# Performance work log

Hardware: AMD Instinct MI355X
Metric: run time of the kernel (lower is better)

## Reference

```python
import jax, jax.numpy as jnp
import numpy as np

TEMPERATURE = 1.0  # spec.temperature, clamped to >=1e-6 in the original
NEG_INF = -1000000000.0


def setup_inputs() -> dict:
    key = jax.random.key(0)
    k_x, k_w1, k_b1, k_w2, k_b2 = jax.random.split(key, 5)
    N, d_in, d_h, E = 32768, 1024, 256, 64
    s1 = 1.0 / np.sqrt(d_in)
    s2 = 1.0 / np.sqrt(d_h)
    return {
        "stage_input": jax.random.normal(k_x, (N, d_in), dtype=jnp.float32),
        "w1": jax.random.uniform(k_w1, (d_in, d_h), jnp.float32, -s1, s1),
        "b1": jax.random.uniform(k_b1, (d_h,), jnp.float32, -s1, s1),
        "w2": jax.random.uniform(k_w2, (d_h, E), jnp.float32, -s2, s2),
        "b2": jax.random.uniform(k_b2, (E,), jnp.float32, -s2, s2),
        "top_k": 8,
    }


def reference(stage_input, w1, b1, w2, b2, top_k):
    # Router MLP: Linear -> ReLU -> (Dropout, eval=identity) -> Linear
    h = jax.nn.relu(stage_input @ w1 + b1)          # [N, d_hidden]
    logits = h @ w2 + b2                             # [N, E]

    scaled = logits / TEMPERATURE
    E = scaled.shape[-1]
    k = min(int(top_k), E)
    if 0 < k < E:
        vals, idx = jax.lax.top_k(scaled, k)         # [N, k]
        rows = jnp.arange(scaled.shape[0])[:, None]
        masked = jnp.full_like(scaled, NEG_INF).at[rows, idx].set(vals)
    else:
        masked = scaled

    probs = jax.nn.softmax(masked, axis=-1)          # [N, E]
    return logits, masked, probs
```

## Files before the change

### kernel.cpp

```cpp
#include <hip/hip_runtime.h>
#include <hip/hip_bf16.h>
#include <float.h>


#define N_ROWS 32768
#define D_IN   1024
#define D_H    256
#define N_E    64
#define NEG_INF_VAL (-1000000000.0f)

typedef _Float16 f16x8 __attribute__((ext_vector_type(8)));
typedef float    f32x4  __attribute__((ext_vector_type(4)));
typedef float    f32x16 __attribute__((ext_vector_type(16)));

#define MM32(A, B, C) __builtin_amdgcn_mfma_f32_32x32x16_f16(A, B, C, 0, 0, 0)
#define MM16(A, B, C) __builtin_amdgcn_mfma_f32_16x16x32_f16(A, B, C, 0, 0, 0)

#define KBAR()                                         \
  do {                                                 \
    asm volatile("s_waitcnt lgkmcnt(0)" ::: "memory"); \
    __builtin_amdgcn_s_barrier();                      \
    asm volatile("" ::: "memory");                     \
  } while (0)

__global__ __launch_bounds__(256) void split_weights_kernel(
    const float* __restrict__ w1, const float* __restrict__ w2,
    _Float16* __restrict__ w1pk_h, _Float16* __restrict__ w1pk_l,
    _Float16* __restrict__ w2pk_h, _Float16* __restrict__ w2pk_l) {
  int idx = blockIdx.x * 256 + threadIdx.x;
  if (idx < D_IN * D_H) {
    const int k = idx >> 8;
    const int n = idx & 255;
    const float v = w1[idx];
    const _Float16 hi = (_Float16)v;
    const _Float16 lo = (_Float16)(v - (float)hi);
    const int wv8 = n >> 5, l31 = n & 31;
    const int it = k >> 6, kf = (k >> 4) & 3, kg = (k >> 3) & 1, j = k & 7;
    const int lane = kg * 32 + l31;
    const int off = (((wv8 * 16 + it) * 4 + kf) * 64 + lane) * 8 + j;
    w1pk_h[off] = hi;
    w1pk_l[off] = lo;
  } else {
    idx -= D_IN * D_H;
    const int k = idx >> 6;
    const int e = idx & 63;
    const float v = w2[idx];
    const _Float16 hi = (_Float16)v;
    const _Float16 lo = (_Float16)(v - (float)hi);
    const int s = k >> 5, kg = (k >> 3) & 3, j = k & 7;
    const int f = e >> 4, cc = e & 15;
    const int lane = kg * 16 + cc;
    const int off = ((s * 4 + f) * 64 + lane) * 8 + j;
    w2pk_h[off] = hi;
    w2pk_l[off] = lo;
  }
}

__global__ __launch_bounds__(512, 2) void fused_router_kernel(
    const float* __restrict__ x, const _Float16* __restrict__ w1pk_h,
    const _Float16* __restrict__ w1pk_l, const float* __restrict__ b1,
    const _Float16* __restrict__ w2pk_h, const _Float16* __restrict__ w2pk_l,
    const float* __restrict__ b2, const int* __restrict__ topk_p,
    float* __restrict__ out_logits, float* __restrict__ out_masked,
    float* __restrict__ out_probs) {
  __shared__ char lds[65536];

  const int t  = threadIdx.x;
  const int m0 = blockIdx.x * 64;

  const int srow = t >> 3;
  const int slot = (t & 7) * 16;
  const int sw   = (srow & 7) << 4;

  const int wv   = t >> 6;
  const int lane = t & 63;
  const int l31  = lane & 31;
  const int kg   = lane >> 5;

  const float* xrowp = x + (size_t)(m0 + srow) * D_IN + (t & 7) * 8;
  const f16x8* bph = (const f16x8*)w1pk_h;
  const f16x8* bpl = (const f16x8*)w1pk_l;

  f32x16 acc0, acc1;
#pragma unroll
  for (int i = 0; i < 16; ++i) { acc0[i] = 0.f; acc1[i] = 0.f; }

  f16x8 uh0, uh1, uh2, uh3, ul0, ul1, ul2, ul3;
  f16x8 vh0, vh1, vh2, vh3, vl0, vl1, vl2, vl3;

#define STAGE_WRITE(bufi, q0, q1)                                            \
  do {                                                                       \
    const float vv[8] = {q0.x, q0.y, q0.z, q0.w, q1.x, q1.y, q1.z, q1.w};    \
    f16x8 hi8, lo8;                                                          \
    _Pragma("unroll") for (int j = 0; j < 8; ++j) {                          \
      const _Float16 hv = (_Float16)vv[j];                                   \
      hi8[j] = hv; lo8[j] = (_Float16)(vv[j] - (float)hv);                   \
    }                                                                        \
    char* bb = lds + (bufi) * 16384 + srow * 256;                            \
    *(f16x8*)(bb + (slot ^ sw)) = hi8;                                       \
    *(f16x8*)(bb + 128 + (slot ^ sw)) = lo8;                                 \
  } while (0)

#define LOAD_B(BH0, BH1, BH2, BH3, BL0, BL1, BL2, BL3, itv)                  \
  do {                                                                       \
    const int ch = (wv * 16 + (itv)) * 256 + lane;                           \
    BH0 = bph[ch + 0 * 64]; BH1 = bph[ch + 1 * 64];                          \
    BH2 = bph[ch + 2 * 64]; BH3 = bph[ch + 3 * 64];                          \
    BL0 = bpl[ch + 0 * 64]; BL1 = bpl[ch + 1 * 64];                          \
    BL2 = bpl[ch + 2 * 64]; BL3 = bpl[ch + 3 * 64];                          \
  } while (0)

#define MFMA_KF(rb, kfv, BH, BL)                                             \
  do {                                                                       \
    const int kb = (kfv) * 32 + kg * 16;                                     \
    const char* ap0 = (rb) + l31 * 256 + (kb ^ ((l31 & 7) << 4));            \
    const char* ap1 = ap0 + 32 * 256;                                        \
    const f16x8 ah0 = *(const f16x8*)(ap0);                                  \
    const f16x8 al0 = *(const f16x8*)(ap0 + 128);                            \
    const f16x8 ah1 = *(const f16x8*)(ap1);                                  \
    const f16x8 al1 = *(const f16x8*)(ap1 + 128);                            \
    acc0 = MM32(al0, BH, acc0); acc1 = MM32(al1, BH, acc1);                  \
    acc0 = MM32(ah0, BL, acc0); acc1 = MM32(ah1, BL, acc1);                  \
    acc0 = MM32(ah0, BH, acc0); acc1 = MM32(ah1, BH, acc1);                  \
  } while (0)

#define GSTEP(ITV, LB, CH0, CH1, CH2, CH3, CL0, CL1, CL2, CL3,               \
              NH0, NH1, NH2, NH3, NL0, NL1, NL2, NL3)                        \
  do {                                                                       \
    float4 p0, p1;                                                           \
    const bool more = (ITV) + 1 < 16;                                        \
    if (more) {                                                              \
      const float4* xp = (const float4*)(xrowp + ((ITV) + 1) * 64);          \
      p0 = xp[0]; p1 = xp[1];                                                \
      LOAD_B(NH0, NH1, NH2, NH3, NL0, NL1, NL2, NL3, (ITV) + 1);             \
    }                                                                        \
    const char* rb = lds + (LB) * 16384;                                     \
    MFMA_KF(rb, 0, CH0, CL0);                                                \
    MFMA_KF(rb, 1, CH1, CL1);                                                \
    MFMA_KF(rb, 2, CH2, CL2);                                                \
    MFMA_KF(rb, 3, CH3, CL3);                                                \
    if (more) STAGE_WRITE(1 - (LB), p0, p1);                                 \
    KBAR();                                                                  \
  } while (0)

  {
    const float4* xp = (const float4*)(xrowp);
    const float4 q0 = xp[0], q1 = xp[1];
    STAGE_WRITE(0, q0, q1);
    LOAD_B(uh0, uh1, uh2, uh3, ul0, ul1, ul2, ul3, 0);
  }
  KBAR();

#pragma unroll
  for (int ii = 0; ii < 8; ++ii) {
    GSTEP(2 * ii, 0, uh0, uh1, uh2, uh3, ul0, ul1, ul2, ul3,
          vh0, vh1, vh2, vh3, vl0, vl1, vl2, vl3);
    GSTEP(2 * ii + 1, 1, vh0, vh1, vh2, vh3, vl0, vl1, vl2, vl3,
          uh0, uh1, uh2, uh3, ul0, ul1, ul2, ul3);
  }

#define EPI(ACC, MF)                                                         \
  do {                                                                       \
    const int colg = wv * 32 + l31;                                          \
    const float bias = b1[colg];                                             \
    _Pragma("unroll") for (int r = 0; r < 16; ++r) {                         \
      const int row = (MF) * 32 + (r & 3) + 8 * (r >> 2) + 4 * kg;           \
      const float hv = fmaxf(ACC[r] + bias, 0.0f);                           \
      const _Float16 hhi = (_Float16)hv;                                     \
      const _Float16 hlo = (_Float16)(hv - (float)hhi);                      \
      const int byo = row * 512 + ((colg * 2) ^ ((row & 7) << 4));           \
      *(_Float16*)(lds + byo) = hhi;                                         \
      *(_Float16*)(lds + 32768 + byo) = hlo;                                 \
    }                                                                        \
  } while (0)

  EPI(acc0, 0); EPI(acc1, 1);
#undef EPI
  KBAR();

  if (wv < 4) {
    const int c   = lane & 15;
    const int kg4 = lane >> 4;
    const int rowl = wv * 16 + c;
    const int sw2 = (rowl & 7) << 4;
    const char* hhb = lds + rowl * 512;
    const char* hlb = lds + 32768 + rowl * 512;
    const f16x8* b2ph = (const f16x8*)w2pk_h;
    const f16x8* b2pl = (const f16x8*)w2pk_l;

    f32x4 r0 = {0.f, 0.f, 0.f, 0.f};
    f32x4 r1 = {0.f, 0.f, 0.f, 0.f};
    f32x4 r2 = {0.f, 0.f, 0.f, 0.f};
    f32x4 r3 = {0.f, 0.f, 0.f, 0.f};

#pragma unroll
    for (int s = 0; s < 8; ++s) {
      const int kb = (s * 64 + kg4 * 16) ^ sw2;
      const f16x8 ah = *(const f16x8*)(hhb + kb);
      const f16x8 al = *(const f16x8*)(hlb + kb);
      const int ch = s * 256 + lane;
      const f16x8 bh0 = b2ph[ch +   0], bh1 = b2ph[ch +  64];
      const f16x8 bh2 = b2ph[ch + 128], bh3 = b2ph[ch + 192];
      const f16x8 bl0 = b2pl[ch +   0], bl1 = b2pl[ch +  64];
      const f16x8 bl2 = b2pl[ch + 128], bl3 = b2pl[ch + 192];
      r0 = MM16(al, bh0, r0); r1 = MM16(al, bh1, r1);
      r2 = MM16(al, bh2, r2); r3 = MM16(al, bh3, r3);
      r0 = MM16(ah, bl0, r0); r1 = MM16(ah, bl1, r1);
      r2 = MM16(ah, bl2, r2); r3 = MM16(ah, bl3, r3);
      r0 = MM16(ah, bh0, r0); r1 = MM16(ah, bh1, r1);
      r2 = MM16(ah, bh2, r2); r3 = MM16(ah, bh3, r3);
    }

    const int K = topk_p[0];
    const bool doMask = (K > 0 && K < N_E);
    const float b2v0 = b2[c], b2v1 = b2[16 + c], b2v2 = b2[32 + c],
                b2v3 = b2[48 + c];
    const int rowbase = m0 + wv * 16;

#pragma unroll
    for (int r = 0; r < 4; ++r) {
      const int row = rowbase + kg4 * 4 + r;
      float* lg = out_logits + (size_t)row * N_E;
      float* mk = out_masked + (size_t)row * N_E;
      float* pb = out_probs  + (size_t)row * N_E;

      const float v0 = r0[r] + b2v0;
      const float v1 = r1[r] + b2v1;
      const float v2 = r2[r] + b2v2;
      const float v3 = r3[r] + b2v3;
      lg[c] = v0; lg[16 + c] = v1; lg[32 + c] = v2; lg[48 + c] = v3;

      bool s0 = true, s1 = true, s2 = true, s3 = true;
      if (doMask) {
        s0 = s1 = s2 = s3 = false;
        float c0 = v0, c1 = v1, c2 = v2, c3 = v3;
        for (int it = 0; it < K; ++it) {
          float m = c0; int mi = c;
          if (c1 > m) { m = c1; mi = 16 + c; }
          if (c2 > m) { m = c2; mi = 32 + c; }
          if (c3 > m) { m = c3; mi = 48 + c; }
#pragma unroll
          for (int off = 1; off <= 8; off <<= 1) {
            const float om = __shfl_xor(m, off);
            const int   oi = __shfl_xor(mi, off);
            if (om > m || (om == m && oi < mi)) { m = om; mi = oi; }
          }
          if ((mi & 15) == c) {
            const int f = mi >> 4;
            s0 = s0 || (f == 0); c0 = (f == 0) ? -FLT_MAX : c0;
            s1 = s1 || (f == 1); c1 = (f == 1) ? -FLT_MAX : c1;
            s2 = s2 || (f == 2); c2 = (f == 2) ? -FLT_MAX : c2;
            s3 = s3 || (f == 3); c3 = (f == 3) ? -FLT_MAX : c3;
          }
        }
      }
      const float m0v = s0 ? v0 : NEG_INF_VAL;
      const float m1v = s1 ? v1 : NEG_INF_VAL;
      const float m2v = s2 ? v2 : NEG_INF_VAL;
      const float m3v = s3 ? v3 : NEG_INF_VAL;
      mk[c] = m0v; mk[16 + c] = m1v; mk[32 + c] = m2v; mk[48 + c] = m3v;

      float mx = fmaxf(fmaxf(m0v, m1v), fmaxf(m2v, m3v));
#pragma unroll
      for (int off = 1; off <= 8; off <<= 1)
        mx = fmaxf(mx, __shfl_xor(mx, off));
      const float e0 = __expf(m0v - mx);
      const float e1 = __expf(m1v - mx);
      const float e2 = __expf(m2v - mx);
      const float e3 = __expf(m3v - mx);
      float sm = e0 + e1 + e2 + e3;
#pragma unroll
      for (int off = 1; off <= 8; off <<= 1) sm += __shfl_xor(sm, off);
      const float inv = 1.0f / sm;
      pb[c] = e0 * inv; pb[16 + c] = e1 * inv; pb[32 + c] = e2 * inv;
      pb[48 + c] = e3 * inv;
    }
  }
#undef GSTEP
#undef MFMA_KF
#undef LOAD_B
#undef STAGE_WRITE
}

extern "C" void kernel_launch(void* const* d_in, const int* in_sizes, int n_in,
                              void* d_out, int out_size, void* d_ws,
                              size_t ws_size, hipStream_t stream) {
  const float* x  = (const float*)d_in[0];
  const float* w1 = (const float*)d_in[1];
  const float* b1 = (const float*)d_in[2];
  const float* w2 = (const float*)d_in[3];
  const float* b2 = (const float*)d_in[4];
  const int* topk = (const int*)d_in[5];

  char* ws = (char*)d_ws;
  _Float16* w1pk_h = (_Float16*)(ws);
  _Float16* w1pk_l = (_Float16*)(ws + 524288);
  _Float16* w2pk_h = (_Float16*)(ws + 1048576);
  _Float16* w2pk_l = (_Float16*)(ws + 1081344);

  float* out_logits = (float*)d_out;
  float* out_masked = out_logits + (size_t)N_ROWS * N_E;
  float* out_probs  = out_masked + (size_t)N_ROWS * N_E;

  split_weights_kernel<<<(D_IN * D_H + D_H * N_E) / 256, 256, 0, stream>>>(
      w1, w2, w1pk_h, w1pk_l, w2pk_h, w2pk_l);

  fused_router_kernel<<<N_ROWS / 64, 512, 0, stream>>>(
      x, w1pk_h, w1pk_l, b1, w2pk_h, w2pk_l, b2, topk, out_logits, out_masked,
      out_probs);
}
```

Baseline: 82.52 us.

## Interleave global prefetch with per-k MFMA phases using barriers and setprio

Restructures the GEMM1 main loop into four phases per K step. Each phase reads its A fragment from LDS, issues part of the next tile's global loads for x and the B fragments, then runs its MFMAs at raised wave priority. Extra s_barriers keep the waves in lockstep, and empty asm statements pin the prefetched values so the loads issue early. Launch bounds go from 2 to 4 waves per SIMD, which caps register usage and may cause spills. The added barriers also add synchronization cost.

```diff
diff --git a/kernel.cpp b/kernel.cpp
--- a/kernel.cpp
+++ b/kernel.cpp
@@ -15,6 +15,13 @@
 
 #define MM32(A, B, C) __builtin_amdgcn_mfma_f32_32x32x16_f16(A, B, C, 0, 0, 0)
 #define MM16(A, B, C) __builtin_amdgcn_mfma_f32_16x16x32_f16(A, B, C, 0, 0, 0)
+
+#define PINX(q) asm volatile("" : : "v"((q).x), "v"((q).y), "v"((q).z), "v"((q).w))
+#define PINB(h)                                                              \
+  do {                                                                       \
+    const f32x4 _f = __builtin_bit_cast(f32x4, (h));                         \
+    asm volatile("" : : "v"(_f[0]), "v"(_f[1]), "v"(_f[2]), "v"(_f[3]));     \
+  } while (0)
 
 #define KBAR()                                         \
   do {                                                 \
@@ -56,7 +63,7 @@
   }
 }
 
-__global__ __launch_bounds__(512, 2) void fused_router_kernel(
+__global__ __launch_bounds__(512, 4) void fused_router_kernel(
     const float* __restrict__ x, const _Float16* __restrict__ w1pk_h,
     const _Float16* __restrict__ w1pk_l, const float* __restrict__ b1,
     const _Float16* __restrict__ w2pk_h, const _Float16* __restrict__ w2pk_l,
@@ -76,6 +83,7 @@
   const int lane = t & 63;
   const int l31  = lane & 31;
   const int kg   = lane >> 5;
+  const int swA  = (l31 & 7) << 4;
 
   const float* xrowp = x + (size_t)(m0 + srow) * D_IN + (t & 7) * 8;
   const f16x8* bph = (const f16x8*)w1pk_h;
@@ -101,53 +109,88 @@
     *(f16x8*)(bb + 128 + (slot ^ sw)) = lo8;                                 \
   } while (0)
 
-#define LOAD_B(BH0, BH1, BH2, BH3, BL0, BL1, BL2, BL3, itv)                  \
-  do {                                                                       \
-    const int ch = (wv * 16 + (itv)) * 256 + lane;                           \
-    BH0 = bph[ch + 0 * 64]; BH1 = bph[ch + 1 * 64];                          \
-    BH2 = bph[ch + 2 * 64]; BH3 = bph[ch + 3 * 64];                          \
-    BL0 = bpl[ch + 0 * 64]; BL1 = bpl[ch + 1 * 64];                          \
-    BL2 = bpl[ch + 2 * 64]; BL3 = bpl[ch + 3 * 64];                          \
-  } while (0)
-
-#define MFMA_KF(rb, kfv, BH, BL)                                             \
-  do {                                                                       \
-    const int kb = (kfv) * 32 + kg * 16;                                     \
-    const char* ap0 = (rb) + l31 * 256 + (kb ^ ((l31 & 7) << 4));            \
-    const char* ap1 = ap0 + 32 * 256;                                        \
-    const f16x8 ah0 = *(const f16x8*)(ap0);                                  \
-    const f16x8 al0 = *(const f16x8*)(ap0 + 128);                            \
-    const f16x8 ah1 = *(const f16x8*)(ap1);                                  \
-    const f16x8 al1 = *(const f16x8*)(ap1 + 128);                            \
-    acc0 = MM32(al0, BH, acc0); acc1 = MM32(al1, BH, acc1);                  \
-    acc0 = MM32(ah0, BL, acc0); acc1 = MM32(ah1, BL, acc1);                  \
-    acc0 = MM32(ah0, BH, acc0); acc1 = MM32(ah1, BH, acc1);                  \
+#define READ_A(rb, KF, AH0, AL0, AH1, AL1)                                   \
+  const char* ap0_##KF = (rb) + l31 * 256 + (((KF)*32 + kg*16) ^ swA);       \
+  const char* ap1_##KF = ap0_##KF + 32 * 256;                                \
+  const f16x8 AH0 = *(const f16x8*)(ap0_##KF);                               \
+  const f16x8 AL0 = *(const f16x8*)(ap0_##KF + 128);                         \
+  const f16x8 AH1 = *(const f16x8*)(ap1_##KF);                               \
+  const f16x8 AL1 = *(const f16x8*)(ap1_##KF + 128)
+
+#define MFMA_PHASE(AH0, AL0, AH1, AL1, BH, BL)                               \
+  do {                                                                       \
+    __builtin_amdgcn_s_setprio(1);                                           \
+    acc0 = MM32(AL0, BH, acc0); acc1 = MM32(AL1, BH, acc1);                  \
+    acc0 = MM32(AH0, BL, acc0); acc1 = MM32(AH1, BL, acc1);                  \
+    acc0 = MM32(AH0, BH, acc0); acc1 = MM32(AH1, BH, acc1);                  \
+    __builtin_amdgcn_s_setprio(0);                                           \
   } while (0)
 
 #define GSTEP(ITV, LB, CH0, CH1, CH2, CH3, CL0, CL1, CL2, CL3,               \
               NH0, NH1, NH2, NH3, NL0, NL1, NL2, NL3)                        \
   do {                                                                       \
-    float4 p0, p1;                                                           \
     const bool more = (ITV) + 1 < 16;                                        \
-    if (more) {                                                              \
-      const float4* xp = (const float4*)(xrowp + ((ITV) + 1) * 64);          \
-      p0 = xp[0]; p1 = xp[1];                                                \
-      LOAD_B(NH0, NH1, NH2, NH3, NL0, NL1, NL2, NL3, (ITV) + 1);             \
-    }                                                                        \
     const char* rb = lds + (LB) * 16384;                                     \
-    MFMA_KF(rb, 0, CH0, CL0);                                                \
-    MFMA_KF(rb, 1, CH1, CL1);                                                \
-    MFMA_KF(rb, 2, CH2, CL2);                                                \
-    MFMA_KF(rb, 3, CH3, CL3);                                                \
-    if (more) STAGE_WRITE(1 - (LB), p0, p1);                                 \
-    KBAR();                                                                  \
+    float4 px0, px1;                                                         \
+                  \
+    {                                                                        \
+      READ_A(rb, 0, ah0, al0, ah1, al1);                                     \
+      if (more) {                                                            \
+        const float4* xp = (const float4*)(xrowp + ((ITV) + 1) * 64);        \
+        px0 = xp[0]; px1 = xp[1];                                            \
+        PINX(px0); PINX(px1);                                                \
+      }                                                                      \
+      __builtin_amdgcn_s_barrier();                                          \
+      MFMA_PHASE(ah0, al0, ah1, al1, CH0, CL0);                              \
+      __builtin_amdgcn_s_barrier();                                          \
+    }                                                                        \
+            \
+    {                                                                        \
+      READ_A(rb, 1, ah0, al0, ah1, al1);                                     \
+      if (more) {                                                            \
+        const int chn = (wv * 16 + (ITV) + 1) * 256 + lane;                  \
+        NH0 = bph[chn + 0 * 64]; NL0 = bpl[chn + 0 * 64];                    \
+        NH1 = bph[chn + 1 * 64]; NL1 = bpl[chn + 1 * 64];                    \
+        PINB(NH0); PINB(NL0); PINB(NH1); PINB(NL1);                          \
+      }                                                                      \
+      __builtin_amdgcn_s_barrier();                                          \
+      MFMA_PHASE(ah0, al0, ah1, al1, CH1, CL1);                              \
+      __builtin_amdgcn_s_barrier();                                          \
+    }                                                                        \
+            \
+    {                                                                        \
+      READ_A(rb, 2, ah0, al0, ah1, al1);                                     \
+      if (more) {                                                            \
+        const int chn = (wv * 16 + (ITV) + 1) * 256 + lane;                  \
+        NH2 = bph[chn + 2 * 64]; NL2 = bpl[chn + 2 * 64];                    \
+        NH3 = bph[chn + 3 * 64]; NL3 = bpl[chn + 3 * 64];                    \
+        PINB(NH2); PINB(NL2); PINB(NH3); PINB(NL3);                          \
+      }                                                                      \
+      __builtin_amdgcn_s_barrier();                                          \
+      MFMA_PHASE(ah0, al0, ah1, al1, CH2, CL2);                              \
+      __builtin_amdgcn_s_barrier();                                          \
+    }                                                                        \
+      \
+    {                                                                        \
+      READ_A(rb, 3, ah0, al0, ah1, al1);                                     \
+      __builtin_amdgcn_s_barrier();                                          \
+      MFMA_PHASE(ah0, al0, ah1, al1, CH3, CL3);                              \
+      if (more) STAGE_WRITE(1 - (LB), px0, px1);                             \
+      KBAR();                                                                \
+    }                                                                        \
   } while (0)
 
   {
     const float4* xp = (const float4*)(xrowp);
     const float4 q0 = xp[0], q1 = xp[1];
     STAGE_WRITE(0, q0, q1);
-    LOAD_B(uh0, uh1, uh2, uh3, ul0, ul1, ul2, ul3, 0);
+    const int ch = (wv * 16 + 0) * 256 + lane;
+    uh0 = bph[ch + 0 * 64]; ul0 = bpl[ch + 0 * 64];
+    uh1 = bph[ch + 1 * 64]; ul1 = bpl[ch + 1 * 64];
+    uh2 = bph[ch + 2 * 64]; ul2 = bpl[ch + 2 * 64];
+    uh3 = bph[ch + 3 * 64]; ul3 = bpl[ch + 3 * 64];
+    PINB(uh0); PINB(ul0); PINB(uh1); PINB(ul1);
+    PINB(uh2); PINB(ul2); PINB(uh3); PINB(ul3);
   }
   KBAR();
 
@@ -277,8 +320,8 @@
     }
   }
 #undef GSTEP
-#undef MFMA_KF
-#undef LOAD_B
+#undef MFMA_PHASE
+#undef READ_A
 #undef STAGE_WRITE
 }
 
```

New measurement: 193.7 us. 135% more time.
